# Kernel optimization log

Measured on AMD Instinct MI355X. Metric: run time of the kernel, lower is better.

## Reference

```python
import jax, jax.numpy as jnp
import numpy as np

EMBED_DIM = 1024
NUM_HEADS = 16
NUM_GLOBAL = 4
NUM_LOCAL = NUM_HEADS - NUM_GLOBAL
WINDOW = 256
HEAD_DIM = EMBED_DIM // NUM_HEADS


def setup_inputs() -> dict:
    key = jax.random.key(0)
    k1, k2, k3 = jax.random.split(key, 3)
    B, S = 4, 2048
    x = jax.random.normal(k1, (B, S, EMBED_DIM), dtype=jnp.float32)
    w_qkv = jax.random.normal(k2, (EMBED_DIM, 3 * EMBED_DIM), dtype=jnp.float32) * (EMBED_DIM ** -0.5)
    b_qkv = jnp.zeros((3 * EMBED_DIM,), dtype=jnp.float32)
    w_out = jax.random.normal(k3, (EMBED_DIM, EMBED_DIM), dtype=jnp.float32) * (EMBED_DIM ** -0.5)
    b_out = jnp.zeros((EMBED_DIM,), dtype=jnp.float32)
    return {"x": x, "w_qkv": w_qkv, "b_qkv": b_qkv, "w_out": w_out, "b_out": b_out}


def _masks(seq_len):
    i = jnp.arange(seq_len)[:, None]
    j = jnp.arange(seq_len)[None, :]
    diff = i - j
    global_mask = diff < 0                      # True = masked (strictly future)
    local_mask = (diff < 0) | (diff > WINDOW)   # True = masked (outside window)
    return global_mask, local_mask


def _attend(q, k, v, mask):
    # q,k,v: [B,h,S,D]; mask: [S,S] True = disallow
    scores = jnp.einsum('bhqd,bhkd->bhqk', q, k) * (HEAD_DIM ** -0.5)
    scores = jnp.where(mask[None, None], -jnp.inf, scores)
    w = jax.nn.softmax(scores, axis=-1)
    return jnp.einsum('bhqk,bhkd->bhqd', w, v)


def reference(x, w_qkv, b_qkv, w_out, b_out):
    B, S, _ = x.shape
    qkv = x @ w_qkv + b_qkv                      # [B,S,3E]
    q, k, v = jnp.split(qkv, 3, axis=-1)
    def heads(t):
        return t.reshape(B, S, NUM_HEADS, HEAD_DIM).transpose(0, 2, 1, 3)
    q, k, v = heads(q), heads(k), heads(v)       # [B,H,S,D]
    gmask, lmask = _masks(S)
    ctx_g = _attend(q[:, :NUM_GLOBAL], k[:, :NUM_GLOBAL], v[:, :NUM_GLOBAL], gmask)
    ctx_l = _attend(q[:, NUM_GLOBAL:], k[:, NUM_GLOBAL:], v[:, NUM_GLOBAL:], lmask)
    ctx = jnp.concatenate([ctx_g, ctx_l], axis=1)          # [B,H,S,D]
    ctx = ctx.transpose(0, 2, 1, 3).reshape(B, S, EMBED_DIM)
    return ctx @ w_out + b_out
```

## Files before the change

### kernel.cpp

```cpp
#include <hip/hip_runtime.h>
#include <stdint.h>

#define EMB 1024
#define SEQ 2048
#define NB 4
#define NH 16
#define HD 64
#define NGLOB 4
#define WIN 256
#define MTOT (NB*SEQ)
#define NQKV (3*EMB)

#define PART_U16 2176
#define NGJOBS 4160
#define NLJOBS 3072

typedef __attribute__((ext_vector_type(8))) short bf16x8;
typedef __attribute__((ext_vector_type(4))) float f32x4;
typedef __attribute__((ext_vector_type(16))) float f32x16;
typedef unsigned short u16;
typedef unsigned int u32;

#define CL2 0.18033688011112042f

#if __has_builtin(__builtin_amdgcn_exp2f)
#define EXP2(x) __builtin_amdgcn_exp2f(x)
#else
#define EXP2(x) exp2f(x)
#endif

__device__ __forceinline__ u16 f2bf(float f) {
  u32 u = __builtin_bit_cast(u32, f);
  u += 0x7fffu + ((u >> 16) & 1u);
  return (u16)(u >> 16);
}

__device__ __forceinline__ float bf2f(u16 v) {
  u32 u = (u32)v << 16;
  return __builtin_bit_cast(float, u);
}

__device__ __forceinline__ u32 packtrunc(float a, float b) {
  u32 ua = __builtin_bit_cast(u32, a);
  u32 ub = __builtin_bit_cast(u32, b);
  return (ua >> 16) | (ub & 0xffff0000u);
}


#define MFMA16(a, b, c) __builtin_amdgcn_mfma_f32_16x16x32_bf16(a, b, c, 0, 0, 0)
#define MFMA32(a, b, c) __builtin_amdgcn_mfma_f32_32x32x16_bf16(a, b, c, 0, 0, 0)
#define GLD16(g, l) __builtin_amdgcn_global_load_lds( \
    (const __attribute__((address_space(1))) void*)(g), \
    (__attribute__((address_space(3))) void*)(l), 16, 0, 0)

__global__ void k_cast(const float* __restrict__ in, u16* __restrict__ out, int n4) {
  int i = blockIdx.x * blockDim.x + threadIdx.x;
  if (i >= n4) return;
  float4 f = ((const float4*)in)[i];
  ushort4 o;
  o.x = f2bf(f.x); o.y = f2bf(f.y); o.z = f2bf(f.z); o.w = f2bf(f.w);
  ((ushort4*)out)[i] = o;
}

__global__ void k_transpose_cast(const float* __restrict__ w, u16* __restrict__ wt,
                                 int R, int C) {
  __shared__ float tile[32][33];
  int c0 = blockIdx.x * 32, r0 = blockIdx.y * 32;
  int tx = threadIdx.x, ty = threadIdx.y;
  #pragma unroll
  for (int j = 0; j < 32; j += 8)
    tile[ty + j][tx] = w[(size_t)(r0 + ty + j) * C + (c0 + tx)];
  __syncthreads();
  #pragma unroll
  for (int j = 0; j < 32; j += 8)
    wt[(size_t)(c0 + ty + j) * R + (r0 + tx)] = f2bf(tile[tx][ty + j]);
}

template <int EPI>
__global__ __launch_bounds__(256, 2) void k_gemm(
    const u16* __restrict__ A, const u16* __restrict__ Bt,
    const float* __restrict__ bias,
    u16* __restrict__ Qo, u16* __restrict__ Ko, u16* __restrict__ Vt,
    float* __restrict__ outp) {
  __shared__ __align__(16) u16 ldsA[128 * 64];
  __shared__ __align__(16) u16 ldsB[128 * 64];
  const int tid = threadIdx.x;
  const int w = tid >> 6, lane = tid & 63;
  const int wm = w >> 1, wn = w & 1;
  const int m0 = blockIdx.x * 128, n0 = blockIdx.y * 128;
  const int rq = lane & 15, g = lane >> 4;

  const int srow = lane >> 3;
  const int scol = ((lane & 7) ^ srow) << 3;

  f32x4 acc[4][4] = {};
  char* ldsAb = (char*)ldsA;
  char* ldsBb = (char*)ldsB;

  for (int k0 = 0; k0 < EMB; k0 += 64) {
    #pragma unroll
    for (int it = 0; it < 4; ++it) {
      int t = w * 4 + it;
      int row = t * 8 + srow;
      GLD16(A + (size_t)(m0 + row) * EMB + k0 + scol, ldsAb + t * 1024);
      GLD16(Bt + (size_t)(n0 + row) * EMB + k0 + scol, ldsBb + t * 1024);
    }
    __syncthreads();
    #pragma unroll
    for (int ks = 0; ks < 2; ++ks) {
      bf16x8 af[4], bfr[4];
      #pragma unroll
      for (int i = 0; i < 4; ++i) {
        int rowA = wm * 64 + i * 16 + rq;
        int off = (ks * 64 + (g << 4)) ^ ((rowA & 7) << 4);
        af[i] = *(const bf16x8*)(ldsAb + rowA * 128 + off);
        int rowB = wn * 64 + i * 16 + rq;
        int offb = (ks * 64 + (g << 4)) ^ ((rowB & 7) << 4);
        bfr[i] = *(const bf16x8*)(ldsBb + rowB * 128 + offb);
      }
      #pragma unroll
      for (int mi = 0; mi < 4; ++mi)
        #pragma unroll
        for (int ni = 0; ni < 4; ++ni)
          acc[mi][ni] = MFMA16(af[mi], bfr[ni], acc[mi][ni]);
    }
    __syncthreads();
  }

  #pragma unroll
  for (int ni = 0; ni < 4; ++ni) {
    int col = n0 + wn * 64 + ni * 16 + rq;
    float bv = bias[col];
    if (EPI == 0) {
      int part = col >> 10;
      int hh = (col & 1023) >> 6;
      int d = col & 63;
      #pragma unroll
      for (int mi = 0; mi < 4; ++mi) {
        #pragma unroll
        for (int i = 0; i < 4; ++i) {
          int m = m0 + wm * 64 + mi * 16 + g * 4 + i;
          int b = m >> 11, s = m & 2047;
          u16 val = f2bf(acc[mi][ni][i] + bv);
          size_t bh = (size_t)(b * NH + hh);
          if (part == 0)      Qo[(bh * SEQ + s) * HD + d] = val;
          else if (part == 1) Ko[(bh * SEQ + s) * HD + d] = val;
          else                Vt[((bh * 128 + (s >> 4)) * 64 + d) * 16 + (s & 15)] = val;
        }
      }
    } else {
      #pragma unroll
      for (int mi = 0; mi < 4; ++mi)
        #pragma unroll
        for (int i = 0; i < 4; ++i) {
          int m = m0 + wm * 64 + mi * 16 + g * 4 + i;
          outp[(size_t)m * EMB + col] = acc[mi][ni][i] + bv;
        }
    }
  }
}

__global__ __launch_bounds__(256, 4) void k_attn(
    const u16* __restrict__ Q, const u16* __restrict__ K,
    const u16* __restrict__ Vt, u16* __restrict__ ctx,
    u16* __restrict__ part) {
  const int w = threadIdx.x >> 6, lane = threadIdx.x & 63;
  const int l31 = lane & 31;
  const int hi = lane >> 5;
  const bool hib = hi != 0;
  const int hi8 = hi * 8, hi4 = hi * 4;

  const int j = blockIdx.x * 4 + w;
  const bool isglob = j < NGJOBS;

  int bh, qt, cstart, clen, band = 0;
  if (isglob) {
    int rem = j, b = 0;
    while (b < 7 && rem >= 144 * (b + 1)) { rem -= 144 * (b + 1); ++b; }
    band = b;
    int nseg = b + 1;
    int qoff = (rem >> 4) / nseg;
    int r2 = rem - qoff * 16 * nseg;
    int seg = r2 >> 4, bg = r2 & 15;
    qt = 9 * b + qoff;
    bh = (bg >> 2) * 16 + (bg & 3);
    int L = qt + 1;
    int base = L / nseg, rm = L - base * nseg;
    clen = base + (seg < rm ? 1 : 0);
    cstart = seg * base + (seg < rm ? seg : rm);
  } else {
    int lidx = j - NGJOBS;
    int bl = lidx >> 6;
    bh = (bl / 12) * 16 + 4 + (bl % 12);
    qt = lidx & 63;
    int qb_ = qt * 32;
    int klo = (qb_ > WIN) ? qb_ - WIN : 0;
    cstart = klo >> 5;
    clen = qt + 1 - cstart;
  }

  const int qb = qt * 32;
  const int h = bh & 15;
  const int b_ = bh >> 4;
  const bool isloc = !isglob;

  const u16* Qp = Q + (size_t)bh * SEQ * HD;
  const u16* Kp = K + (size_t)bh * SEQ * HD;
  const u16* Vp = Vt + (size_t)bh * SEQ * HD;

  const int q = qb + l31;
  const float NINF = -__builtin_inff();

  bf16x8 qf[4];
  #pragma unroll
  for (int jj = 0; jj < 4; ++jj)
    qf[jj] = *(const bf16x8*)(Qp + (size_t)q * HD + jj * 16 + hi8);

  f32x16 oacc[2] = {};
  float m = NINF;
  float l = 0.f;

  int kc = cstart * 32;
  #pragma unroll 2
  for (int it = 0; it < clen; ++it, kc += 32) {
    bf16x8 kf0, kf1, kf2, kf3, vf[2][2];
    {
      const u16* Kr = Kp + (size_t)(kc + l31) * HD + hi8;
      kf0 = *(const bf16x8*)(Kr);
      kf1 = *(const bf16x8*)(Kr + 16);
      kf2 = *(const bf16x8*)(Kr + 32);
      kf3 = *(const bf16x8*)(Kr + 48);
      const u16* Vb = Vp + (size_t)(kc >> 4) * 1024 + hi8;
      #pragma unroll
      for (int dt = 0; dt < 2; ++dt)
        #pragma unroll
        for (int sl = 0; sl < 2; ++sl)
          vf[dt][sl] = *(const bf16x8*)(Vb + (sl * 64 + dt * 32 + l31) * 16);
    }

    f32x16 s0 = {}, s1 = {};
    s0 = MFMA32(kf0, qf[0], s0);
    s1 = MFMA32(kf2, qf[2], s1);
    s0 = MFMA32(kf1, qf[1], s0);
    s1 = MFMA32(kf3, qf[3], s1);

    const bool needs_mask = (kc == qb) || (isloc && (qb - kc > 225));
    float p[16];
    float cmax = NINF;
    if (needs_mask) {
      #pragma unroll
      for (int r = 0; r < 16; ++r) {
        int key = kc + hi4 + (r & 3) + 8 * (r >> 2);
        float v = s0[r] + s1[r];
        bool bad = (key > q) || (isloc && (q - key > WIN));
        p[r] = bad ? NINF : v;
        cmax = fmaxf(cmax, p[r]);
      }
    } else {
      #pragma unroll
      for (int r = 0; r < 16; ++r) {
        p[r] = s0[r] + s1[r];
        cmax = fmaxf(cmax, p[r]);
      }
    }
    cmax = fmaxf(cmax, __shfl_xor(cmax, 32));

    float muC;
    if (__any(cmax > m + 64.f)) {
      float mn = fmaxf(m, cmax);
      muC = (mn == NINF) ? 0.f : mn * CL2;
      float oldC = (m == NINF) ? muC : m * CL2;
      float f = EXP2(oldC - muC);
      m = mn;
      l *= f;
      #pragma unroll
      for (int dt = 0; dt < 2; ++dt)
        #pragma unroll
        for (int r = 0; r < 16; ++r)
          oacc[dt][r] *= f;
    } else {
      muC = (m == NINF) ? 0.f : m * CL2;
    }

    float psum = 0.f;
    #pragma unroll
    for (int r = 0; r < 16; ++r) {
      float e = EXP2(__builtin_fmaf(p[r], CL2, -muC));
      p[r] = e;
      psum += e;
    }
    psum += __shfl_xor(psum, 32);
    l += psum;

    union { u32 u[4]; bf16x8 v; } pbf[2];
    #pragma unroll
    for (int sl = 0; sl < 2; ++sl) {
      int s8 = sl * 8;
      u32 X0 = packtrunc(p[s8 + 0], p[s8 + 1]);
      u32 X1 = packtrunc(p[s8 + 2], p[s8 + 3]);
      u32 X2 = packtrunc(p[s8 + 4], p[s8 + 5]);
      u32 X3 = packtrunc(p[s8 + 6], p[s8 + 7]);
      u32 oX0 = (u32)__shfl_xor((int)X0, 32);
      u32 oX1 = (u32)__shfl_xor((int)X1, 32);
      u32 oX2 = (u32)__shfl_xor((int)X2, 32);
      u32 oX3 = (u32)__shfl_xor((int)X3, 32);
      pbf[sl].u[0] = hib ? oX2 : X0;
      pbf[sl].u[1] = hib ? oX3 : X1;
      pbf[sl].u[2] = hib ? X2 : oX0;
      pbf[sl].u[3] = hib ? X3 : oX1;
    }

    #pragma unroll
    for (int dt = 0; dt < 2; ++dt)
      #pragma unroll
      for (int sl = 0; sl < 2; ++sl)
        oacc[dt] = MFMA32(vf[dt][sl], pbf[sl].v, oacc[dt]);
  }

  if (isglob && band != 0) {
    u16* PB = part + (size_t)j * PART_U16;
    #pragma unroll
    for (int dt = 0; dt < 2; ++dt)
      #pragma unroll
      for (int r = 0; r < 16; ++r) {
        int d = dt * 32 + hi4 + (r & 3) + 8 * (r >> 2);
        PB[d * 32 + l31] = f2bf(oacc[dt][r]);
      }
    float* PF = (float*)(PB + 2048);
    if (hi == 0) { PF[l31] = m; PF[32 + l31] = l; }
  } else {
    float linv = 1.f / l;
    #pragma unroll
    for (int dt = 0; dt < 2; ++dt) {
      #pragma unroll
      for (int r = 0; r < 16; ++r) {
        int d = dt * 32 + hi4 + (r & 3) + 8 * (r >> 2);
        int e = h * HD + d;
        ctx[(size_t)(b_ * SEQ + q) * EMB + e] = f2bf(oacc[dt][r] * linv);
      }
    }
  }
}

__global__ __launch_bounds__(256, 4) void k_merge(
    const u16* __restrict__ part, u16* __restrict__ ctx) {
  const int t = blockIdx.x;
  const int bg = t & 15;
  const int qt = t >> 4;
  const int band = qt / 9;
  const int nseg = band + 1;
  if (nseg == 1) return;
  const int jbase = 72 * band * (band + 1) + (qt - 9 * band) * 16 * nseg + bg;
  const int bh = (bg >> 2) * 16 + (bg & 3);
  const int qb = qt * 32;
  const int h = bh & 15;
  const int bb = bh >> 4;

  __shared__ u16 ob[64][34];
  __shared__ float fml[8][64];

  const int tid = threadIdx.x;
  for (int e = tid; e < nseg * 64; e += 256) {
    int s = e >> 6, k = e & 63;
    fml[s][k] = ((const float*)(part + (size_t)(jbase + s * 16) * PART_U16 + 2048))[k];
  }
  __syncthreads();

  const int dd = tid & 63;
  const int qg = tid >> 6;
  float M[8], Lsum[8], val[8];
  #pragma unroll
  for (int i = 0; i < 8; ++i) {
    int qq = qg * 8 + i;
    float mx = fml[0][qq];
    for (int s = 1; s < nseg; ++s) mx = fmaxf(mx, fml[s][qq]);
    M[i] = mx; Lsum[i] = 0.f; val[i] = 0.f;
  }

  for (int s = 0; s < nseg; ++s) {
    __syncthreads();
    const u32* src = (const u32*)(part + (size_t)(jbase + s * 16) * PART_U16);
    #pragma unroll
    for (int c = 0; c < 4; ++c) {
      int wd = tid * 4 + c;
      *(u32*)&ob[wd >> 4][(wd & 15) * 2] = src[wd];
    }
    __syncthreads();
    #pragma unroll
    for (int i = 0; i < 8; ++i) {
      int qq = qg * 8 + i;
      float wgt = EXP2((fml[s][qq] - M[i]) * CL2);
      Lsum[i] += wgt * fml[s][32 + qq];
      val[i] += wgt * bf2f(ob[dd][qq]);
    }
  }

  #pragma unroll
  for (int i = 0; i < 8; ++i) {
    int qq = qg * 8 + i;
    ctx[(size_t)(bb * SEQ + (qb + qq)) * EMB + h * HD + dd] = f2bf(val[i] / Lsum[i]);
  }
}

extern "C" void kernel_launch(void* const* d_in, const int* in_sizes, int n_in,
                              void* d_out, int out_size, void* d_ws, size_t ws_size,
                              hipStream_t stream) {
  const float* x     = (const float*)d_in[0];
  const float* w_qkv = (const float*)d_in[1];
  const float* b_qkv = (const float*)d_in[2];
  const float* w_out = (const float*)d_in[3];
  const float* b_out = (const float*)d_in[4];
  float* out = (float*)d_out;

  char* ws = (char*)d_ws;
  u16* xb    = (u16*)(ws);
  u16* wqkvT = (u16*)(ws + (16ull << 20));
  u16* woutT = (u16*)(ws + (22ull << 20));
  u16* Qb    = (u16*)(ws + (24ull << 20));
  u16* Kb    = (u16*)(ws + (40ull << 20));
  u16* Vt    = (u16*)(ws + (56ull << 20));
  u16* ctx   = (u16*)(ws + (72ull << 20));
  u16* part  = xb;

  k_cast<<<(MTOT * EMB / 4) / 256, 256, 0, stream>>>(x, xb, MTOT * EMB / 4);
  dim3 tb(32, 8);
  k_transpose_cast<<<dim3(NQKV / 32, EMB / 32), tb, 0, stream>>>(w_qkv, wqkvT, EMB, NQKV);
  k_transpose_cast<<<dim3(EMB / 32, EMB / 32), tb, 0, stream>>>(w_out, woutT, EMB, EMB);

  k_gemm<0><<<dim3(MTOT / 128, NQKV / 128), 256, 0, stream>>>(
      xb, wqkvT, b_qkv, Qb, Kb, Vt, nullptr);

  k_attn<<<dim3((NGJOBS + NLJOBS) / 4), 256, 0, stream>>>(Qb, Kb, Vt, ctx, part);
  k_merge<<<dim3(1024), 256, 0, stream>>>(part, ctx);

  k_gemm<1><<<dim3(MTOT / 128, EMB / 128), 256, 0, stream>>>(
      ctx, woutT, b_out, nullptr, nullptr, nullptr, out);
}
```

Baseline: 197.3 us.

## Remap attention job indices so each XCD handles fixed batch-heads

Reorders how attention jobs map to blocks. The low 3 bits of the block id (likely the XCD under round-robin dispatch) now select a fixed pair of global batch-heads, or six local batch-heads, so each XCD's K/V working set stays in its own L2. Partial-result slots are renumbered per batch-head and the merge kernel's indexing is updated to match. The risk is worse load balance or tail effects, because the job order across time changes.

```diff
diff --git a/kernel.cpp b/kernel.cpp
--- a/kernel.cpp
+++ b/kernel.cpp
@@ -12,8 +12,7 @@
 #define NQKV (3*EMB)
 
 #define PART_U16 2176
-#define NGJOBS 4160
-#define NLJOBS 3072
+#define JOBS_PER_BG 260
 
 typedef __attribute__((ext_vector_type(8))) short bf16x8;
 typedef __attribute__((ext_vector_type(4))) float f32x4;
@@ -170,29 +169,37 @@
   const bool hib = hi != 0;
   const int hi8 = hi * 8, hi4 = hi * 4;
 
-  const int j = blockIdx.x * 4 + w;
-  const bool isglob = j < NGJOBS;
-
-  int bh, qt, cstart, clen, band = 0;
+  const int gid = blockIdx.x;
+  const int x = gid & 7;
+  const int jb = gid >> 3;
+  const bool isglob = jb < 130;
+
+  int bh, qt, cstart, clen, band = 0, slot = 0;
   if (isglob) {
-    int rem = j, b = 0;
-    while (b < 7 && rem >= 144 * (b + 1)) { rem -= 144 * (b + 1); ++b; }
+    int pk = jb * 4 + w;
+    int bg = 2 * x + (pk >= JOBS_PER_BG);
+    int r = (pk >= JOBS_PER_BG) ? pk - JOBS_PER_BG : pk;
+    int b = 0;
+    while (b < 7 && r >= 9 * (b + 1) * (b + 2) / 2) ++b;
     band = b;
+    int rb = r - 9 * b * (b + 1) / 2;
     int nseg = b + 1;
-    int qoff = (rem >> 4) / nseg;
-    int r2 = rem - qoff * 16 * nseg;
-    int seg = r2 >> 4, bg = r2 & 15;
+    if (b == 7) nseg = 8;
+    int qoff = rb / nseg;
+    int seg = rb - qoff * nseg;
     qt = 9 * b + qoff;
     bh = (bg >> 2) * 16 + (bg & 3);
+    slot = bg * JOBS_PER_BG + r;
     int L = qt + 1;
     int base = L / nseg, rm = L - base * nseg;
     clen = base + (seg < rm ? 1 : 0);
     cstart = seg * base + (seg < rm ? seg : rm);
   } else {
-    int lidx = j - NGJOBS;
-    int bl = lidx >> 6;
+    int lj = (jb - 130) * 4 + w;
+    int bls = lj >> 6;
+    int bl = 6 * x + bls;
+    qt = lj & 63;
     bh = (bl / 12) * 16 + 4 + (bl % 12);
-    qt = lidx & 63;
     int qb_ = qt * 32;
     int klo = (qb_ > WIN) ? qb_ - WIN : 0;
     cstart = klo >> 5;
@@ -318,7 +325,7 @@
   }
 
   if (isglob && band != 0) {
-    u16* PB = part + (size_t)j * PART_U16;
+    u16* PB = part + (size_t)slot * PART_U16;
     #pragma unroll
     for (int dt = 0; dt < 2; ++dt)
       #pragma unroll
@@ -350,7 +357,8 @@
   const int band = qt / 9;
   const int nseg = band + 1;
   if (nseg == 1) return;
-  const int jbase = 72 * band * (band + 1) + (qt - 9 * band) * 16 * nseg + bg;
+  const int jbase = bg * JOBS_PER_BG + 9 * band * (band + 1) / 2
+                    + (qt - 9 * band) * nseg;
   const int bh = (bg >> 2) * 16 + (bg & 3);
   const int qb = qt * 32;
   const int h = bh & 15;
@@ -362,7 +370,7 @@
   const int tid = threadIdx.x;
   for (int e = tid; e < nseg * 64; e += 256) {
     int s = e >> 6, k = e & 63;
-    fml[s][k] = ((const float*)(part + (size_t)(jbase + s * 16) * PART_U16 + 2048))[k];
+    fml[s][k] = ((const float*)(part + (size_t)(jbase + s) * PART_U16 + 2048))[k];
   }
   __syncthreads();
 
@@ -379,7 +387,7 @@
 
   for (int s = 0; s < nseg; ++s) {
     __syncthreads();
-    const u32* src = (const u32*)(part + (size_t)(jbase + s * 16) * PART_U16);
+    const u32* src = (const u32*)(part + (size_t)(jbase + s) * PART_U16);
     #pragma unroll
     for (int c = 0; c < 4; ++c) {
       int wd = tid * 4 + c;
@@ -430,7 +438,7 @@
   k_gemm<0><<<dim3(MTOT / 128, NQKV / 128), 256, 0, stream>>>(
       xb, wqkvT, b_qkv, Qb, Kb, Vt, nullptr);
 
-  k_attn<<<dim3((NGJOBS + NLJOBS) / 4), 256, 0, stream>>>(Qb, Kb, Vt, ctx, part);
+  k_attn<<<dim3(226 * 8), 256, 0, stream>>>(Qb, Kb, Vt, ctx, part);
   k_merge<<<dim3(1024), 256, 0, stream>>>(part, ctx);
 
   k_gemm<1><<<dim3(MTOT / 128, EMB / 128), 256, 0, stream>>>(
```

New measurement: 197.1 us. About the same (-0.1%).
